# Kernel optimization log

Hardware: AMD Instinct MI355X
Metric: run time of the kernel (lower is better)

## Reference

```python
import math
import jax, jax.numpy as jnp
import numpy as np


def fht(x):
    """Normalized fast Hadamard transform over the last axis (size = power of 2)."""
    n = x.shape[-1]
    pre = x.shape[:-1]
    y = x.reshape(-1, n)
    h = 1
    while h < n:
        y = y.reshape(-1, n // (2 * h), 2, h)
        a = y[:, :, 0, :]
        b = y[:, :, 1, :]
        y = jnp.stack([a + b, a - b], axis=2)
        h *= 2
    return y.reshape(*pre, n) * jnp.float32(1.0 / math.sqrt(n))


def setup_inputs() -> dict:
    key = jax.random.key(0)
    ks = jax.random.split(key, 8)
    B, N, M, G = 8192, 4096, 4096, 512  # tokens, in_features(n_pad), out_features(m_pad), n_pad//8
    CB = 256  # E8 shell codebook entries (8-bit indices), each an 8-dim lattice point
    x = jax.random.normal(ks[0], (B, N), dtype=jnp.float32)
    Qidxs = jax.random.randint(ks[1], (M, G), 0, CB, dtype=jnp.int32)
    Qidxs2 = jax.random.randint(ks[2], (M, G), 0, CB, dtype=jnp.int32)
    SU = jax.random.rademacher(ks[3], (M,), dtype=jnp.float32)  # row sign vector
    SV = jax.random.rademacher(ks[4], (N,), dtype=jnp.float32)  # column sign vector
    codebook = jax.random.normal(ks[5], (CB, 8), dtype=jnp.float32)
    codebook2 = jax.random.normal(ks[6], (CB, 8), dtype=jnp.float32)
    Wscale = jnp.asarray(0.85, dtype=jnp.float32)
    inv_resid_scale = jnp.asarray(0.07, dtype=jnp.float32)  # nonzero -> stage-2 enabled
    return {"x": x, "Qidxs": Qidxs, "Qidxs2": Qidxs2, "SU": SU, "SV": SV,
            "codebook": codebook, "codebook2": codebook2,
            "Wscale": Wscale, "inv_resid_scale": inv_resid_scale}


def reference(x, Qidxs, Qidxs2, SU, SV, codebook, codebook2, Wscale, inv_resid_scale):
    # in_features == n_pad and out_features == m_pad here (powers of 2), so no pad/slice.
    m_pad, g = Qidxs.shape
    n_pad = g * 8
    # 1) input RHT: signs then Hadamard
    x_rht = fht(x * SV[None, :])  # (B, n_pad)
    # 2) dequantize weights in RHT domain: codebook lookup per 8-dim group + residual stage
    W_rht = codebook[Qidxs].reshape(m_pad, n_pad)
    W_rht = W_rht + codebook2[Qidxs2].reshape(m_pad, n_pad) * inv_resid_scale
    # 3) matmul in RHT domain with global scale
    y_rht = (x_rht @ W_rht.T) * Wscale  # (B, m_pad)
    # 4) output inverse RHT: Hadamard then signs
    y = fht(y_rht) * SU[None, :]
    return y
```

## Files before the change

### kernel.cpp

```cpp
#include <hip/hip_runtime.h>

#define B_DIM 8192
#define N_DIM 4096
#define M_DIM 4096
#define G_DIM 512

typedef short bf16x8 __attribute__((ext_vector_type(8)));
typedef float f32x4 __attribute__((ext_vector_type(4)));

typedef __attribute__((address_space(1))) const void gvoid_t;
typedef __attribute__((address_space(3))) void lvoid_t;

__device__ __forceinline__ void load_lds16(const void* g, void* l) {
    __builtin_amdgcn_global_load_lds((gvoid_t*)g, (lvoid_t*)l, 16, 0, 0);
}

__device__ __forceinline__ unsigned short f2bf(float f) {
    union { float f; unsigned int u; } v; v.f = f;
    unsigned int u = v.u;
    unsigned int r = (u + 0x7fffu + ((u >> 16) & 1u)) >> 16;
    return (unsigned short)r;
}
__device__ __forceinline__ float bf2f(unsigned short s) {
    union { unsigned int u; float f; } v; v.u = ((unsigned int)s) << 16;
    return v.f;
}

__device__ __forceinline__ void h16(float* v) {
#pragma unroll
    for (int h = 1; h < 16; h <<= 1) {
#pragma unroll
        for (int i = 0; i < 16; i++) {
            if (!(i & h)) {
                float a = v[i], b = v[i | h];
                v[i] = a + b;
                v[i | h] = a - b;
            }
        }
    }
}

__device__ __forceinline__ void h64(float* v) {
#pragma unroll
    for (int h = 1; h < 64; h <<= 1) {
#pragma unroll
        for (int i = 0; i < 64; i++) {
            if (!(i & h)) {
                float a = v[i], b = v[i | h];
                v[i] = a + b;
                v[i | h] = a - b;
            }
        }
    }
}

__global__ __launch_bounds__(256) void k_build_w(
    const int* __restrict__ q1, const int* __restrict__ q2,
    const float* __restrict__ cb1, const float* __restrict__ cb2,
    const float* __restrict__ wsp, const float* __restrict__ irsp,
    unsigned short* __restrict__ W) {
    __shared__ float c1[256 * 9];
    __shared__ float c2[256 * 9];
    int t = threadIdx.x;
#pragma unroll
    for (int j = 0; j < 8; j++) {
        c1[t * 9 + j] = cb1[t * 8 + j];
        c2[t * 9 + j] = cb2[t * 8 + j];
    }
    __syncthreads();
    float ws = wsp[0];
    float irs = irsp[0] * ws;
    int gid = blockIdx.x * 256 + t;
    int i1 = q1[gid] * 9;
    int i2 = q2[gid] * 9;
    union { unsigned short s[8]; int4 v; } o;
#pragma unroll
    for (int j = 0; j < 8; j++) {
        o.s[j] = f2bf(c1[i1 + j] * ws + c2[i2 + j] * irs);
    }
    *(int4*)(W + (size_t)gid * 8) = o.v;
}

__global__ __launch_bounds__(256) void k_hadw(
    unsigned short* __restrict__ W, int base_mul, int step, float scale) {
    int c = blockIdx.x * 256 + threadIdx.x;
    int base = blockIdx.y * base_mul;
    float v[64];
#pragma unroll
    for (int j = 0; j < 64; j++)
        v[j] = bf2f(W[(size_t)(base + j * step) * N_DIM + c]);
    h64(v);
#pragma unroll
    for (int j = 0; j < 64; j++)
        W[(size_t)(base + j * step) * N_DIM + c] = f2bf(v[j] * scale);
}

__global__ __launch_bounds__(256) void k_rht_in(
    const float* __restrict__ x, const float* __restrict__ SV,
    unsigned short* __restrict__ out) {
    __shared__ float lds[4352];
    int row = blockIdx.x;
    int t = threadIdx.x;
    const float* xr = x + (size_t)row * N_DIM;
    float v[16];
#pragma unroll
    for (int r = 0; r < 16; r++) {
        int n = t + (r << 8);
        v[r] = xr[n] * SV[n] * 0.015625f;
    }
    h16(v);
#pragma unroll
    for (int r = 0; r < 16; r++) { int n = t + (r << 8); lds[n + (n >> 4)] = v[r]; }
    __syncthreads();
#pragma unroll
    for (int r = 0; r < 16; r++) { int n = (t << 4) + r; v[r] = lds[n + (n >> 4)]; }
    h16(v);
#pragma unroll
    for (int r = 0; r < 16; r++) { int n = (t << 4) + r; lds[n + (n >> 4)] = v[r]; }
    __syncthreads();
#pragma unroll
    for (int r = 0; r < 16; r++) {
        int n = (t & 15) | (r << 4) | ((t >> 4) << 8);
        v[r] = lds[n + (n >> 4)];
    }
    h16(v);
#pragma unroll
    for (int r = 0; r < 16; r++) {
        int n = (t & 15) | (r << 4) | ((t >> 4) << 8);
        lds[n + (n >> 4)] = v[r];
    }
    __syncthreads();
    unsigned short* orow = out + (size_t)row * N_DIM;
#pragma unroll
    for (int r = 0; r < 16; r++) {
        int n = t + (r << 8);
        orow[n] = f2bf(lds[n + (n >> 4)]);
    }
}

__global__ __launch_bounds__(256) void k_gemm(
    const unsigned short* __restrict__ A,
    const unsigned short* __restrict__ Bw,
    const float* __restrict__ SU,
    float* __restrict__ C) {
    __shared__ __align__(16) unsigned short As[128 * 32];
    __shared__ __align__(16) unsigned short Bs[128 * 32];
    int t = threadIdx.x;
    int w = t >> 6;
    int l = t & 63;
    int bn = blockIdx.x;
    int bm = blockIdx.y;

    int srow = w * 32 + (l >> 2);
    int scol = (l & 3) * 8;
    const unsigned short* ga0 = A + (size_t)(bm * 128 + srow) * N_DIM + scol;
    const unsigned short* ga1 = ga0 + (size_t)16 * N_DIM;
    const unsigned short* gb0 = Bw + (size_t)(bn * 128 + srow) * N_DIM + scol;
    const unsigned short* gb1 = gb0 + (size_t)16 * N_DIM;
    unsigned short* la0 = &As[(w * 32) * 32];
    unsigned short* la1 = &As[(w * 32 + 16) * 32];
    unsigned short* lb0 = &Bs[(w * 32) * 32];
    unsigned short* lb1 = &Bs[(w * 32 + 16) * 32];

    int wm = (w & 1) << 6;
    int wn = (w >> 1) << 6;
    int quad = l >> 4;
    int ln = l & 15;

    const unsigned short* arp[4];
    const unsigned short* brp[4];
#pragma unroll
    for (int i = 0; i < 4; i++) arp[i] = &As[(wm + i * 16 + ln) * 32 + quad * 8];
#pragma unroll
    for (int j = 0; j < 4; j++) brp[j] = &Bs[(wn + j * 16 + ln) * 32 + quad * 8];

    f32x4 acc[4][4];
#pragma unroll
    for (int i = 0; i < 4; i++)
#pragma unroll
        for (int j = 0; j < 4; j++) {
            f32x4 z = {0.f, 0.f, 0.f, 0.f};
            acc[i][j] = z;
        }

    for (int kk = 0; kk < N_DIM / 32; kk++) {
        load_lds16(ga0, la0);
        load_lds16(ga1, la1);
        load_lds16(gb0, lb0);
        load_lds16(gb1, lb1);
        ga0 += 32; ga1 += 32; gb0 += 32; gb1 += 32;
        __syncthreads();
        bf16x8 af[4], bfr[4];
#pragma unroll
        for (int i = 0; i < 4; i++) af[i] = *(const bf16x8*)arp[i];
#pragma unroll
        for (int j = 0; j < 4; j++) bfr[j] = *(const bf16x8*)brp[j];
#pragma unroll
        for (int i = 0; i < 4; i++)
#pragma unroll
            for (int j = 0; j < 4; j++)
                acc[i][j] = __builtin_amdgcn_mfma_f32_16x16x32_bf16(
                    af[i], bfr[j], acc[i][j], 0, 0, 0);
        __syncthreads();
    }

#pragma unroll
    for (int j = 0; j < 4; j++) {
        int col = bn * 128 + wn + j * 16 + ln;
        float su = SU[col];
#pragma unroll
        for (int i = 0; i < 4; i++) {
#pragma unroll
            for (int r = 0; r < 4; r++) {
                int rowg = bm * 128 + wm + i * 16 + quad * 4 + r;
                C[(size_t)rowg * M_DIM + col] = acc[i][j][r] * su;
            }
        }
    }
}

extern "C" void kernel_launch(void* const* d_in, const int* in_sizes, int n_in,
                              void* d_out, int out_size, void* d_ws, size_t ws_size,
                              hipStream_t stream) {
    const float* x    = (const float*)d_in[0];
    const int*   q1   = (const int*)d_in[1];
    const int*   q2   = (const int*)d_in[2];
    const float* SU   = (const float*)d_in[3];
    const float* SV   = (const float*)d_in[4];
    const float* cb1  = (const float*)d_in[5];
    const float* cb2  = (const float*)d_in[6];
    const float* wsp  = (const float*)d_in[7];
    const float* irsp = (const float*)d_in[8];
    float* out = (float*)d_out;

    unsigned short* xrht = (unsigned short*)d_ws;
    unsigned short* Wb   = xrht + (size_t)B_DIM * N_DIM;

    k_build_w<<<dim3((M_DIM * G_DIM) / 256), dim3(256), 0, stream>>>(
        q1, q2, cb1, cb2, wsp, irsp, Wb);
    k_hadw<<<dim3(N_DIM / 256, 64), dim3(256), 0, stream>>>(Wb, 1, 64, 1.0f);
    k_hadw<<<dim3(N_DIM / 256, 64), dim3(256), 0, stream>>>(Wb, 64, 1, 0.015625f);
    k_rht_in<<<dim3(B_DIM), dim3(256), 0, stream>>>(x, SV, xrht);
    k_gemm<<<dim3(M_DIM / 128, B_DIM / 128), dim3(256), 0, stream>>>(
        xrht, Wb, SU, out);
}
```

Measured before the change: 611.8 us.

## Rework GEMM into 256x256 tiles with 4-stage async LDS pipeline and swizzle

Measured after the change: 516.3 us. -15.6%, faster.

```diff
diff --git a/kernel.cpp b/kernel.cpp
--- a/kernel.cpp
+++ b/kernel.cpp
@@ -13,6 +13,10 @@
 
 __device__ __forceinline__ void load_lds16(const void* g, void* l) {
     __builtin_amdgcn_global_load_lds((gvoid_t*)g, (lvoid_t*)l, 16, 0, 0);
+}
+
+__device__ __forceinline__ unsigned lds_u32(const void* p) {
+    return (unsigned)(unsigned long long)(lvoid_t*)p;
 }
 
 __device__ __forceinline__ unsigned short f2bf(float f) {
@@ -138,85 +142,119 @@
     }
 }
 
-__global__ __launch_bounds__(256) void k_gemm(
+#define DSR(D, A, OFF) \
+    asm volatile("ds_read_b128 %0, %1 offset:" #OFF : "=v"(D) : "v"(A))
+
+__global__ __launch_bounds__(512, 2) void k_gemm(
     const unsigned short* __restrict__ A,
     const unsigned short* __restrict__ Bw,
     const float* __restrict__ SU,
     float* __restrict__ C) {
-    __shared__ __align__(16) unsigned short As[128 * 32];
-    __shared__ __align__(16) unsigned short Bs[128 * 32];
+    __shared__ __align__(16) unsigned short lds[4 * 16384];
+
     int t = threadIdx.x;
     int w = t >> 6;
     int l = t & 63;
-    int bn = blockIdx.x;
-    int bm = blockIdx.y;
-
-    int srow = w * 32 + (l >> 2);
-    int scol = (l & 3) * 8;
-    const unsigned short* ga0 = A + (size_t)(bm * 128 + srow) * N_DIM + scol;
-    const unsigned short* ga1 = ga0 + (size_t)16 * N_DIM;
-    const unsigned short* gb0 = Bw + (size_t)(bn * 128 + srow) * N_DIM + scol;
-    const unsigned short* gb1 = gb0 + (size_t)16 * N_DIM;
-    unsigned short* la0 = &As[(w * 32) * 32];
-    unsigned short* la1 = &As[(w * 32 + 16) * 32];
-    unsigned short* lb0 = &Bs[(w * 32) * 32];
-    unsigned short* lb1 = &Bs[(w * 32 + 16) * 32];
-
-    int wm = (w & 1) << 6;
-    int wn = (w >> 1) << 6;
+
+    int lin = blockIdx.x;
+    int xcd = lin & 7;
+    int idx = lin >> 3;
+    int bn = xcd * 2 + (idx >> 5);
+    int bm = idx & 31;
+
+    int lx = l ^ (l >> 3);
+    const unsigned short* aS0 =
+        A + (size_t)(bm * 256 + w * 16 + (lx >> 2)) * N_DIM + (lx & 3) * 8;
+    const unsigned short* aS1 = aS0 + (size_t)128 * N_DIM;
+    const unsigned short* bS0 =
+        Bw + (size_t)(bn * 256 + w * 16 + (lx >> 2)) * N_DIM + (lx & 3) * 8;
+    const unsigned short* bS1 = bS0 + (size_t)128 * N_DIM;
+
+    int wm = w >> 2;
+    int wn = w & 3;
     int quad = l >> 4;
     int ln = l & 15;
-
-    const unsigned short* arp[4];
-    const unsigned short* brp[4];
-#pragma unroll
-    for (int i = 0; i < 4; i++) arp[i] = &As[(wm + i * 16 + ln) * 32 + quad * 8];
-#pragma unroll
-    for (int j = 0; j < 4; j++) brp[j] = &Bs[(wn + j * 16 + ln) * 32 + quad * 8];
-
-    f32x4 acc[4][4];
-#pragma unroll
-    for (int i = 0; i < 4; i++)
+    unsigned ldsU = lds_u32(lds);
+    unsigned aBase = ldsU +
+        (unsigned)(((((wm * 128) + ln) << 6) | (quad << 4)) ^ ((ln >> 1) << 4));
+    unsigned bBase = ldsU + 16384u +
+        (unsigned)(((((wn * 64) + ln) << 6) | (quad << 4)) ^ ((ln >> 1) << 4));
+
+    f32x4 acc[8][4];
+#pragma unroll
+    for (int i = 0; i < 8; i++)
 #pragma unroll
         for (int j = 0; j < 4; j++) {
             f32x4 z = {0.f, 0.f, 0.f, 0.f};
             acc[i][j] = z;
         }
 
-    for (int kk = 0; kk < N_DIM / 32; kk++) {
-        load_lds16(ga0, la0);
-        load_lds16(ga1, la1);
-        load_lds16(gb0, lb0);
-        load_lds16(gb1, lb1);
-        ga0 += 32; ga1 += 32; gb0 += 32; gb1 += 32;
-        __syncthreads();
-        bf16x8 af[4], bfr[4];
-#pragma unroll
-        for (int i = 0; i < 4; i++) af[i] = *(const bf16x8*)arp[i];
-#pragma unroll
-        for (int j = 0; j < 4; j++) bfr[j] = *(const bf16x8*)brp[j];
-#pragma unroll
-        for (int i = 0; i < 4; i++)
+#define STAGE(KT) do {                                              \
+        int kt_ = (KT);                                             \
+        int ks_ = kt_ < 127 ? kt_ : 127;                            \
+        unsigned short* d_ = lds + ((unsigned)kt_ & 3u) * 16384 + w * 512; \
+        const unsigned short* sa0_ = aS0 + ks_ * 32;                \
+        const unsigned short* sa1_ = aS1 + ks_ * 32;                \
+        const unsigned short* sb0_ = bS0 + ks_ * 32;                \
+        const unsigned short* sb1_ = bS1 + ks_ * 32;                \
+        load_lds16(sa0_, d_);                                       \
+        load_lds16(sa1_, d_ + 4096);                                \
+        load_lds16(sb0_, d_ + 8192);                                \
+        load_lds16(sb1_, d_ + 12288);                               \
+    } while (0)
+
+    STAGE(0);
+    STAGE(1);
+    STAGE(2);
+
+    for (int k = 0; k < N_DIM / 32; k++) {
+        asm volatile("s_waitcnt vmcnt(8)");
+        __builtin_amdgcn_s_barrier();
+        STAGE(k + 3);
+
+        unsigned au = aBase + (unsigned)(k & 3) * 32768u;
+        unsigned bu = bBase + (unsigned)(k & 3) * 32768u;
+        bf16x8 af[8], bfr[4];
+        DSR(af[0], au, 0);
+        DSR(af[1], au, 1024);
+        DSR(af[2], au, 2048);
+        DSR(af[3], au, 3072);
+        DSR(af[4], au, 4096);
+        DSR(af[5], au, 5120);
+        DSR(af[6], au, 6144);
+        DSR(af[7], au, 7168);
+        DSR(bfr[0], bu, 0);
+        DSR(bfr[1], bu, 1024);
+        DSR(bfr[2], bu, 2048);
+        DSR(bfr[3], bu, 3072);
+        asm volatile("s_waitcnt lgkmcnt(0)");
+        __builtin_amdgcn_sched_barrier(0);
+
+        __builtin_amdgcn_s_setprio(1);
+#pragma unroll
+        for (int i = 0; i < 8; i++)
 #pragma unroll
             for (int j = 0; j < 4; j++)
                 acc[i][j] = __builtin_amdgcn_mfma_f32_16x16x32_bf16(
                     af[i], bfr[j], acc[i][j], 0, 0, 0);
-        __syncthreads();
-    }
+        __builtin_amdgcn_s_setprio(0);
+    }
+    asm volatile("s_waitcnt vmcnt(0)");
 
 #pragma unroll
     for (int j = 0; j < 4; j++) {
-        int col = bn * 128 + wn + j * 16 + ln;
+        int col = bn * 256 + wn * 64 + j * 16 + ln;
         float su = SU[col];
 #pragma unroll
-        for (int i = 0; i < 4; i++) {
+        for (int i = 0; i < 8; i++) {
 #pragma unroll
             for (int r = 0; r < 4; r++) {
-                int rowg = bm * 128 + wm + i * 16 + quad * 4 + r;
+                int rowg = bm * 256 + wm * 128 + i * 16 + quad * 4 + r;
                 C[(size_t)rowg * M_DIM + col] = acc[i][j][r] * su;
             }
         }
     }
+#undef STAGE
 }
 
 extern "C" void kernel_launch(void* const* d_in, const int* in_sizes, int n_in,
@@ -241,6 +279,5 @@
     k_hadw<<<dim3(N_DIM / 256, 64), dim3(256), 0, stream>>>(Wb, 1, 64, 1.0f);
     k_hadw<<<dim3(N_DIM / 256, 64), dim3(256), 0, stream>>>(Wb, 64, 1, 0.015625f);
     k_rht_in<<<dim3(B_DIM), dim3(256), 0, stream>>>(x, SV, xrht);
-    k_gemm<<<dim3(M_DIM / 128, B_DIM / 128), dim3(256), 0, stream>>>(
-        xrht, Wb, SU, out);
-}
+    k_gemm<<<dim3(512), dim3(512), 0, stream>>>(xrht, Wb, SU, out);
+}
```
